# Kernel optimization log

Hardware: AMD Instinct MI355X
Metric: run time of the kernel (lower is better)

Reference implementation:

```python
import jax, jax.numpy as jnp
import numpy as np

# RadixAttention EXTEND forward: queries over newly-extended tokens attend to
# (a) the full cached prefix KV (non-causal) and (b) the extend-token KV (causal),
# equivalent to attention over concat([prefix, extend]) with a shifted causal mask.

SCALING = 0.08838834764831845  # 1/sqrt(128)


def setup_inputs() -> dict:
    key = jax.random.key(0)
    k1, k2, k3, k4, k5 = jax.random.split(key, 5)
    B, E, P, H, Hk, D = 4, 512, 1536, 32, 8, 128
    return {
        "q": jax.random.normal(k1, (B, E, H, D), dtype=jnp.float32),
        "k": jax.random.normal(k2, (B, E, Hk, D), dtype=jnp.float32),
        "v": jax.random.normal(k3, (B, E, Hk, D), dtype=jnp.float32),
        "k_cache": jax.random.normal(k4, (B, P, Hk, D), dtype=jnp.float32),
        "v_cache": jax.random.normal(k5, (B, P, Hk, D), dtype=jnp.float32),
    }


def reference(q, k, v, k_cache, v_cache):
    B, E, H, D = q.shape
    Hk = k.shape[2]
    P = k_cache.shape[1]
    g = H // Hk  # GQA group size
    S = P + E

    k_all = jnp.concatenate([k_cache, k], axis=1)  # [B, S, Hk, D]
    v_all = jnp.concatenate([v_cache, v], axis=1)  # [B, S, Hk, D]

    qg = q.reshape(B, E, Hk, g, D)
    # scores: [B, Hk, g, E, S]
    scores = jnp.einsum("bekgd,bskd->bkges", qg, k_all) * SCALING

    # key j visible to extend-query e iff j <= P + e (prefix fully visible, extend causal)
    visible = jnp.arange(S)[None, :] <= (P + jnp.arange(E))[:, None]  # [E, S]
    scores = jnp.where(visible[None, None, None, :, :], scores, jnp.float32(-1e30))

    p = jax.nn.softmax(scores, axis=-1)
    o = jnp.einsum("bkges,bskd->bekgd", p, v_all).reshape(B, E, H, D)
    # module returns flat [num_tokens, H*D]
    return o.reshape(B * E, H * D)
```

## Files before the change

kernel.cpp:

```cpp
#include <hip/hip_runtime.h>
#include <hip/hip_bf16.h>
#include <stdint.h>
#include <stddef.h>


#define B_ 4
#define E_ 512
#define P_ 1536
#define H_ 32
#define HK_ 8
#define D_ 128
#define G_ 4
#define S_ 2048

#define BLOCK_E 32
#define NT 64
#define PPITCH 72
#define TPITCH 72
#define KVSTRIDE (HK_ * D_)
#define NTHREADS 256
#define M_FIX 12.0f
#define TILE_SHORTS 8192

typedef __attribute__((ext_vector_type(8))) short short8v;
typedef __attribute__((ext_vector_type(4))) float floatx4;

__device__ __forceinline__ short2 f2bf2(float a, float b) {
  __hip_bfloat162 h = __float22bfloat162_rn(float2{a, b});
  return *(short2*)&h;
}
__device__ __forceinline__ short f2bf(float f) {
  union { float f; uint32_t u; } x; x.f = f;
  uint32_t r = x.u + 0x7FFFu + ((x.u >> 16) & 1u);
  return (short)(r >> 16);
}
__device__ __forceinline__ short8v cvt8(const float4 a, const float4 b) {
  short2 p0 = f2bf2(a.x, a.y), p1 = f2bf2(a.z, a.w);
  short2 p2 = f2bf2(b.x, b.y), p3 = f2bf2(b.z, b.w);
  short8v f;
  f[0] = p0.x; f[1] = p0.y; f[2] = p1.x; f[3] = p1.y;
  f[4] = p2.x; f[5] = p2.y; f[6] = p3.x; f[7] = p3.y;
  return f;
}

__global__ __launch_bounds__(256)
void prep_kv(const float* __restrict__ kc, const float* __restrict__ ke,
             const float* __restrict__ vc, const float* __restrict__ ve,
             short* __restrict__ kb, short* __restrict__ vt) {
  __shared__ short TT[D_ * TPITCH];
  const int bid = blockIdx.x;
  const int tid = threadIdx.x;
  if (bid < 4096) {
    const int cid = bid * 256 + tid;
    const int cl  = cid & 15;
    const int j   = (cid >> 4) & (S_ - 1);
    const int kh  = (cid >> 15) & 7;
    const int b   = cid >> 18;
    const float* src = (j < P_)
        ? (kc + (((size_t)b * P_ + j) * HK_ + kh) * D_ + cl * 8)
        : (ke + (((size_t)b * E_ + (j - P_)) * HK_ + kh) * D_ + cl * 8);
    const float4 x0 = *(const float4*)src;
    const float4 x1 = *(const float4*)(src + 4);
    const int t = j >> 6, key = j & 63;
    const int cs = ((cl & 7) ^ (key & 7)) | (cl & 8);
    *(short8v*)&kb[(((size_t)(b * 8 + kh) * 32 + t)) * TILE_SHORTS + key * 128 + cs * 8] =
        cvt8(x0, x1);
  } else {
    const int b2 = bid - 4096;
    const int j0 = (b2 & 31) * 64;
    const int kh = (b2 >> 5) & 7;
    const int b  = b2 >> 8;
#pragma unroll
    for (int it = 0; it < 8; ++it) {
      const int linear = it * 256 + tid;
      const int key = linear >> 5;
      const int dof = (linear & 31) * 4;
      const int j = j0 + key;
      const float* src = (j < P_)
          ? (vc + (((size_t)b * P_ + j) * HK_ + kh) * D_ + dof)
          : (ve + (((size_t)b * E_ + (j - P_)) * HK_ + kh) * D_ + dof);
      const float4 x = *(const float4*)src;
      short2 a = f2bf2(x.x, x.y), c = f2bf2(x.z, x.w);
      TT[(dof + 0) * TPITCH + key] = a.x;
      TT[(dof + 1) * TPITCH + key] = a.y;
      TT[(dof + 2) * TPITCH + key] = c.x;
      TT[(dof + 3) * TPITCH + key] = c.y;
    }
    __syncthreads();
#pragma unroll
    for (int it = 0; it < 4; ++it) {
      const int linear = it * 256 + tid;
      const int d  = linear >> 3;
      const int ck = linear & 7;
      const int cks = ck ^ (d & 7);
      *(short8v*)&vt[(((size_t)(b * 8 + kh) * 32 + (j0 >> 6))) * TILE_SHORTS + d * 64 + cks * 8] =
          *(const short8v*)&TT[d * TPITCH + ck * 8];
    }
  }
}

__global__ __launch_bounds__(NTHREADS, 2)
void radix_attn(const float* __restrict__ q,
                const short* __restrict__ kb,
                const short* __restrict__ vt,
                float* __restrict__ out) {
  __shared__ short KT[2][NT * D_];
  __shared__ short VTs[2][D_ * NT];
  __shared__ short PW[4][16 * PPITCH];

  const int flat = blockIdx.x;
  const int kh   = flat & 7;
  const int b    = (flat >> 3) & 3;
  const int e0   = (flat >> 5) * BLOCK_E;
  const int tid  = threadIdx.x;
  const int wave = tid >> 6;
  const int lane = tid & 63;
  const int quad = lane >> 4;
  const int l16  = lane & 15;
  const int h    = kh * G_ + wave;

  short8v qf[2][4];
#pragma unroll
  for (int rb = 0; rb < 2; ++rb) {
    const int e = e0 + rb * 16 + l16;
    const float* qp = q + (((size_t)b * E_ + e) * H_ + h) * D_ + quad * 8;
#pragma unroll
    for (int kcc = 0; kcc < 4; ++kcc)
      qf[rb][kcc] = cvt8(*(const float4*)(qp + kcc * 32), *(const float4*)(qp + kcc * 32 + 4));
  }

  short8v ones8;
#pragma unroll
  for (int i = 0; i < 8; ++i) ones8[i] = (l16 == 0) ? (short)0x3F80 : (short)0;

  floatx4 oacc[2][8];
#pragma unroll
  for (int rb = 0; rb < 2; ++rb)
#pragma unroll
    for (int dt = 0; dt < 8; ++dt) oacc[rb][dt] = (floatx4){0.f, 0.f, 0.f, 0.f};
  floatx4 acc_l[2] = {(floatx4){0.f, 0.f, 0.f, 0.f}, (floatx4){0.f, 0.f, 0.f, 0.f}};

  const short* kbt = kb + (size_t)(b * 8 + kh) * 32 * TILE_SHORTS;
  const short* vtt = vt + (size_t)(b * 8 + kh) * 32 * TILE_SHORTS;

  const int slimit = P_ + e0 + BLOCK_E;
  const int ntiles = (slimit + NT - 1) / NT;
  const float sc = 0.08838834764831845f * 1.44269504088896340f;

  auto dma = [&](int t, int buf) {
    const char* kg = (const char*)kbt + (size_t)t * 16384 + wave * 4096 + lane * 16;
    const char* vg = (const char*)vtt + (size_t)t * 16384 + wave * 4096 + lane * 16;
    short* kl = &KT[buf][wave * 2048];
    short* vl = &VTs[buf][wave * 2048];
#pragma unroll
    for (int g = 0; g < 4; ++g) {
      __builtin_amdgcn_global_load_lds(
          (const __attribute__((address_space(1))) void*)(kg + g * 1024),
          (__attribute__((address_space(3))) void*)(kl + g * 512), 16, 0, 0);
      __builtin_amdgcn_global_load_lds(
          (const __attribute__((address_space(1))) void*)(vg + g * 1024),
          (__attribute__((address_space(3))) void*)(vl + g * 512), 16, 0, 0);
    }
  };

  dma(0, 0);

  for (int t = 0; t < ntiles; ++t) {
    const int kt0 = t * NT;
    const int cur = t & 1;

    __syncthreads();
    if (t + 1 < ntiles) dma(t + 1, cur ^ 1);

    floatx4 sfr[2][4];
#pragma unroll
    for (int nc = 0; nc < 4; ++nc) {
      short8v kf[4];
#pragma unroll
      for (int kcc = 0; kcc < 4; ++kcc) {
        const int cl = kcc * 4 + quad;
        const int cs = ((cl & 7) ^ (l16 & 7)) | (cl & 8);
        kf[kcc] = *(const short8v*)&KT[cur][(nc * 16 + l16) * D_ + cs * 8];
      }
#pragma unroll
      for (int rb = 0; rb < 2; ++rb) {
        floatx4 acc = (floatx4){0.f, 0.f, 0.f, 0.f};
#pragma unroll
        for (int kcc = 0; kcc < 4; ++kcc)
          acc = __builtin_amdgcn_mfma_f32_16x16x32_bf16(kf[kcc], qf[rb][kcc], acc, 0, 0, 0);
        sfr[rb][nc] = acc;
      }
    }

    short8v vfr[2][4];
#pragma unroll
    for (int kc = 0; kc < 2; ++kc)
#pragma unroll
      for (int dt = 0; dt < 4; ++dt) {
        const int cs = (kc * 4 + quad) ^ (l16 & 7);
        vfr[kc][dt] = *(const short8v*)&VTs[cur][(dt * 16 + l16) * NT + cs * 8];
      }

    short8v pf[2][2];
#pragma unroll
    for (int rb = 0; rb < 2; ++rb) {
      const bool need_mask = (kt0 + NT - 1 > P_ + e0 + rb * 16);
      const int qlim = P_ + e0 + rb * 16 + l16;
#pragma unroll
      for (int nc = 0; nc < 4; ++nc) {
        float p[4];
#pragma unroll
        for (int reg = 0; reg < 4; ++reg) {
          float pe = __builtin_amdgcn_exp2f(__builtin_fmaf(sfr[rb][nc][reg], sc, -M_FIX));
          if (need_mask) {
            const int jkey = kt0 + nc * 16 + quad * 4 + reg;
            if (jkey > qlim) pe = 0.f;
          }
          p[reg] = pe;
        }
        const short2 a = f2bf2(p[0], p[1]), c = f2bf2(p[2], p[3]);
        short4 y; y.x = a.x; y.y = a.y; y.z = c.x; y.w = c.y;
        *(short4*)&PW[wave][l16 * PPITCH + nc * 16 + quad * 4] = y;
      }
#pragma unroll
      for (int kc = 0; kc < 2; ++kc)
        pf[rb][kc] = *(const short8v*)&PW[wave][l16 * PPITCH + kc * 32 + quad * 8];
    }

#pragma unroll
    for (int kc = 0; kc < 2; ++kc) {
#pragma unroll
      for (int dt = 0; dt < 8; ++dt) {
        short8v vf;
        if (dt < 4) {
          vf = vfr[kc][dt];
        } else {
          const int cs = (kc * 4 + quad) ^ (l16 & 7);
          vf = *(const short8v*)&VTs[cur][(dt * 16 + l16) * NT + cs * 8];
        }
#pragma unroll
        for (int rb = 0; rb < 2; ++rb)
          oacc[rb][dt] = __builtin_amdgcn_mfma_f32_16x16x32_bf16(pf[rb][kc], vf, oacc[rb][dt], 0, 0, 0);
      }
#pragma unroll
      for (int rb = 0; rb < 2; ++rb)
        acc_l[rb] = __builtin_amdgcn_mfma_f32_16x16x32_bf16(pf[rb][kc], ones8, acc_l[rb], 0, 0, 0);
    }
  }

#pragma unroll
  for (int rb = 0; rb < 2; ++rb) {
    float inv[4];
#pragma unroll
    for (int reg = 0; reg < 4; ++reg) {
      const float l = __shfl(acc_l[rb][reg], lane & 48, 64);
      inv[reg] = 1.0f / l;
    }
#pragma unroll
    for (int reg = 0; reg < 4; ++reg) {
      const int erow = e0 + rb * 16 + quad * 4 + reg;
      float* op = out + (size_t)(b * E_ + erow) * (H_ * D_) + h * D_ + l16;
#pragma unroll
      for (int dt = 0; dt < 8; ++dt)
        op[dt * 16] = oacc[rb][dt][reg] * inv[reg];
    }
  }
}

__global__ __launch_bounds__(1024, 4)
void radix_attn_fp32(const float* __restrict__ q,
                     const float* __restrict__ ke,
                     const float* __restrict__ ve,
                     const float* __restrict__ kc,
                     const float* __restrict__ vc,
                     float* __restrict__ out) {
  __shared__ short KT[NT * 136];
  __shared__ short VTs[D_ * TPITCH];
  __shared__ short PW[16][16 * 80];
  const int flat = blockIdx.x;
  const int kh = flat & 7, b = (flat >> 3) & 3, e0 = (flat >> 5) * 64;
  const int tid = threadIdx.x, wave = tid >> 6, lane = tid & 63;
  const int quad = lane >> 4, l16 = lane & 15;
  const int gi = wave & 3, rbw = wave >> 2, h = kh * G_ + gi;
  short8v qf[4];
  {
    const int e = e0 + rbw * 16 + l16;
    const float* qp = q + (((size_t)b * E_ + e) * H_ + h) * D_ + quad * 8;
#pragma unroll
    for (int kcc = 0; kcc < 4; ++kcc)
      qf[kcc] = cvt8(*(const float4*)(qp + kcc * 32), *(const float4*)(qp + kcc * 32 + 4));
  }
  short8v ones8;
#pragma unroll
  for (int i = 0; i < 8; ++i) ones8[i] = (l16 == 0) ? (short)0x3F80 : (short)0;
  floatx4 oacc[8];
#pragma unroll
  for (int d = 0; d < 8; ++d) oacc[d] = (floatx4){0.f, 0.f, 0.f, 0.f};
  floatx4 acc_l = (floatx4){0.f, 0.f, 0.f, 0.f};
  float mrow[4];
#pragma unroll
  for (int r = 0; r < 4; ++r) mrow[r] = -1e30f;
  const float* kcb = kc + (size_t)b * P_ * KVSTRIDE + (size_t)kh * D_;
  const float* keb = ke + (size_t)b * E_ * KVSTRIDE + (size_t)kh * D_;
  const float* vcb = vc + (size_t)b * P_ * KVSTRIDE + (size_t)kh * D_;
  const float* veb = ve + (size_t)b * E_ * KVSTRIDE + (size_t)kh * D_;
  const int ntiles = (P_ + e0 + 64) / NT;
  const float sc = 0.08838834764831845f * 1.44269504088896340f;
  for (int t = 0; t < ntiles; ++t) {
    const int kt0 = t * NT;
    __syncthreads();
#pragma unroll
    for (int it = 0; it < 2; ++it) {
      const int linear = it * 1024 + tid;
      const int key = linear >> 5, dof = (linear & 31) * 4;
      const int j = kt0 + key;
      const float* src = (j < P_) ? (kcb + (size_t)j * KVSTRIDE) : (keb + (size_t)(j - P_) * KVSTRIDE);
      const float4 x = *(const float4*)(src + dof);
      short2 a = f2bf2(x.x, x.y), c = f2bf2(x.z, x.w);
      short4 y; y.x = a.x; y.y = a.y; y.z = c.x; y.w = c.y;
      *(short4*)&KT[key * 136 + dof] = y;
    }
#pragma unroll
    for (int it = 0; it < 2; ++it) {
      const int linear = it * 1024 + tid;
      const int key = linear & 63, dg = (linear >> 6) * 4;
      const int j = kt0 + key;
      const float* src = (j < P_) ? (vcb + (size_t)j * KVSTRIDE) : (veb + (size_t)(j - P_) * KVSTRIDE);
      const float4 x = *(const float4*)(src + dg);
      short2 a = f2bf2(x.x, x.y), c = f2bf2(x.z, x.w);
      VTs[(dg + 0) * TPITCH + key] = a.x;
      VTs[(dg + 1) * TPITCH + key] = a.y;
      VTs[(dg + 2) * TPITCH + key] = c.x;
      VTs[(dg + 3) * TPITCH + key] = c.y;
    }
    __syncthreads();
    floatx4 sfr[4];
#pragma unroll
    for (int nc = 0; nc < 4; ++nc) {
      floatx4 acc = (floatx4){0.f, 0.f, 0.f, 0.f};
#pragma unroll
      for (int kcc = 0; kcc < 4; ++kcc) {
        const short8v bf = *(const short8v*)&KT[(nc * 16 + l16) * 136 + kcc * 32 + quad * 8];
        acc = __builtin_amdgcn_mfma_f32_16x16x32_bf16(qf[kcc], bf, acc, 0, 0, 0);
      }
      sfr[nc] = acc;
    }
    const bool need_mask = (kt0 + NT - 1 > P_ + e0 + rbw * 16);
#pragma unroll
    for (int nc = 0; nc < 4; ++nc)
#pragma unroll
      for (int reg = 0; reg < 4; ++reg) {
        float s = sfr[nc][reg] * sc;
        if (need_mask) {
          const int jkey = kt0 + nc * 16 + l16;
          const int erow = e0 + rbw * 16 + quad * 4 + reg;
          if (jkey > P_ + erow) s = -1e30f;
        }
        sfr[nc][reg] = s;
      }
    float mt[4];
#pragma unroll
    for (int reg = 0; reg < 4; ++reg)
      mt[reg] = fmaxf(fmaxf(sfr[0][reg], sfr[1][reg]), fmaxf(sfr[2][reg], sfr[3][reg]));
#pragma unroll
    for (int off = 1; off < 16; off <<= 1)
#pragma unroll
      for (int reg = 0; reg < 4; ++reg)
        mt[reg] = fmaxf(mt[reg], __shfl_xor(mt[reg], off, 64));
#pragma unroll
    for (int reg = 0; reg < 4; ++reg) {
      const float mnew = fmaxf(mrow[reg], mt[reg]);
      const float alpha = __builtin_amdgcn_exp2f(mrow[reg] - mnew);
      mrow[reg] = mnew;
      acc_l[reg] *= alpha;
#pragma unroll
      for (int d = 0; d < 8; ++d) oacc[d][reg] *= alpha;
    }
#pragma unroll
    for (int nc = 0; nc < 4; ++nc)
#pragma unroll
      for (int reg = 0; reg < 4; ++reg) {
        const float p = __builtin_amdgcn_exp2f(sfr[nc][reg] - mrow[reg]);
        PW[wave][(quad * 4 + reg) * 80 + nc * 16 + l16] = f2bf(p);
      }
    const short8v pf0 = *(const short8v*)&PW[wave][l16 * 80 + quad * 8];
    const short8v pf1 = *(const short8v*)&PW[wave][l16 * 80 + 32 + quad * 8];
#pragma unroll
    for (int d = 0; d < 8; ++d) {
      const short8v vf0 = *(const short8v*)&VTs[(d * 16 + l16) * TPITCH + quad * 8];
      const short8v vf1 = *(const short8v*)&VTs[(d * 16 + l16) * TPITCH + 32 + quad * 8];
      oacc[d] = __builtin_amdgcn_mfma_f32_16x16x32_bf16(pf0, vf0, oacc[d], 0, 0, 0);
      oacc[d] = __builtin_amdgcn_mfma_f32_16x16x32_bf16(pf1, vf1, oacc[d], 0, 0, 0);
    }
    acc_l = __builtin_amdgcn_mfma_f32_16x16x32_bf16(pf0, ones8, acc_l, 0, 0, 0);
    acc_l = __builtin_amdgcn_mfma_f32_16x16x32_bf16(pf1, ones8, acc_l, 0, 0, 0);
  }
  float inv[4];
#pragma unroll
  for (int reg = 0; reg < 4; ++reg)
    inv[reg] = 1.0f / __shfl(acc_l[reg], lane & 48, 64);
#pragma unroll
  for (int reg = 0; reg < 4; ++reg) {
    const int erow = e0 + rbw * 16 + quad * 4 + reg;
    float* op = out + (size_t)(b * E_ + erow) * (H_ * D_) + h * D_ + l16;
#pragma unroll
    for (int d = 0; d < 8; ++d)
      op[d * 16] = oacc[d][reg] * inv[reg];
  }
}

extern "C" void kernel_launch(void* const* d_in, const int* in_sizes, int n_in,
                              void* d_out, int out_size, void* d_ws, size_t ws_size,
                              hipStream_t stream) {
  const float* q  = (const float*)d_in[0];
  const float* ke = (const float*)d_in[1];
  const float* ve = (const float*)d_in[2];
  const float* kc = (const float*)d_in[3];
  const float* vc = (const float*)d_in[4];
  float* out = (float*)d_out;

  const size_t kv_shorts = (size_t)B_ * HK_ * S_ * D_;
  const size_t need = 2 * kv_shorts * sizeof(short);

  if (ws_size >= need) {
    short* kb = (short*)d_ws;
    short* vt = kb + kv_shorts;
    prep_kv<<<dim3(4096 + 1024), dim3(256), 0, stream>>>(kc, ke, vc, ve, kb, vt);
    const int nblk = (E_ / BLOCK_E) * HK_ * B_;
    radix_attn<<<dim3(nblk), dim3(NTHREADS), 0, stream>>>(q, kb, vt, out);
  } else {
    radix_attn_fp32<<<dim3(8 * 8 * 4), dim3(1024), 0, stream>>>(q, ke, ve, kc, vc, out);
  }
}
```

Measured before the change: 213.6 us.

## Split row blocks across 8 waves per block and swizzle P scratch

Doubles the block to 512 threads so each wave handles one head and one 16-row slice instead of two slices. This halves per-wave accumulator registers so more waves can be resident (launch bound raised to 4). It also spreads the K/V DMA over 8 waves, XOR-swizzles the P staging buffer instead of padding it, adds s_setprio around the MFMA sections, and unrolls the tile loop by two so the buffer index is a compile-time constant. In exchange, each K fragment loaded from LDS now feeds only one row block, which doubles LDS read traffic per MFMA.

```diff
diff --git a/kernel.cpp b/kernel.cpp
--- a/kernel.cpp
+++ b/kernel.cpp
@@ -15,10 +15,9 @@
 
 #define BLOCK_E 32
 #define NT 64
-#define PPITCH 72
 #define TPITCH 72
 #define KVSTRIDE (HK_ * D_)
-#define NTHREADS 256
+#define NTHREADS 512
 #define M_FIX 12.0f
 #define TILE_SHORTS 8192
 
@@ -99,14 +98,14 @@
   }
 }
 
-__global__ __launch_bounds__(NTHREADS, 2)
+__global__ __launch_bounds__(NTHREADS, 4)
 void radix_attn(const float* __restrict__ q,
                 const short* __restrict__ kb,
                 const short* __restrict__ vt,
                 float* __restrict__ out) {
   __shared__ short KT[2][NT * D_];
   __shared__ short VTs[2][D_ * NT];
-  __shared__ short PW[4][16 * PPITCH];
+  __shared__ short PW[8][1024];
 
   const int flat = blockIdx.x;
   const int kh   = flat & 7;
@@ -117,28 +116,27 @@
   const int lane = tid & 63;
   const int quad = lane >> 4;
   const int l16  = lane & 15;
-  const int h    = kh * G_ + wave;
-
-  short8v qf[2][4];
-#pragma unroll
-  for (int rb = 0; rb < 2; ++rb) {
+  const int gi   = wave & 3;
+  const int rb   = wave >> 2;
+  const int h    = kh * G_ + gi;
+
+  short8v qf[4];
+  {
     const int e = e0 + rb * 16 + l16;
     const float* qp = q + (((size_t)b * E_ + e) * H_ + h) * D_ + quad * 8;
 #pragma unroll
     for (int kcc = 0; kcc < 4; ++kcc)
-      qf[rb][kcc] = cvt8(*(const float4*)(qp + kcc * 32), *(const float4*)(qp + kcc * 32 + 4));
+      qf[kcc] = cvt8(*(const float4*)(qp + kcc * 32), *(const float4*)(qp + kcc * 32 + 4));
   }
 
   short8v ones8;
 #pragma unroll
   for (int i = 0; i < 8; ++i) ones8[i] = (l16 == 0) ? (short)0x3F80 : (short)0;
 
-  floatx4 oacc[2][8];
-#pragma unroll
-  for (int rb = 0; rb < 2; ++rb)
-#pragma unroll
-    for (int dt = 0; dt < 8; ++dt) oacc[rb][dt] = (floatx4){0.f, 0.f, 0.f, 0.f};
-  floatx4 acc_l[2] = {(floatx4){0.f, 0.f, 0.f, 0.f}, (floatx4){0.f, 0.f, 0.f, 0.f}};
+  floatx4 oacc[8];
+#pragma unroll
+  for (int dt = 0; dt < 8; ++dt) oacc[dt] = (floatx4){0.f, 0.f, 0.f, 0.f};
+  floatx4 acc_l = (floatx4){0.f, 0.f, 0.f, 0.f};
 
   const short* kbt = kb + (size_t)(b * 8 + kh) * 32 * TILE_SHORTS;
   const short* vtt = vt + (size_t)(b * 8 + kh) * 32 * TILE_SHORTS;
@@ -147,13 +145,17 @@
   const int ntiles = (slimit + NT - 1) / NT;
   const float sc = 0.08838834764831845f * 1.44269504088896340f;
 
+  const int qlim = P_ + e0 + rb * 16 + l16;
+  const int pb   = l16 * 64;
+  const int swz  = l16 & 7;
+
   auto dma = [&](int t, int buf) {
-    const char* kg = (const char*)kbt + (size_t)t * 16384 + wave * 4096 + lane * 16;
-    const char* vg = (const char*)vtt + (size_t)t * 16384 + wave * 4096 + lane * 16;
-    short* kl = &KT[buf][wave * 2048];
-    short* vl = &VTs[buf][wave * 2048];
-#pragma unroll
-    for (int g = 0; g < 4; ++g) {
+    const char* kg = (const char*)kbt + (size_t)t * 16384 + wave * 2048 + lane * 16;
+    const char* vg = (const char*)vtt + (size_t)t * 16384 + wave * 2048 + lane * 16;
+    short* kl = &KT[buf][wave * 1024];
+    short* vl = &VTs[buf][wave * 1024];
+#pragma unroll
+    for (int g = 0; g < 2; ++g) {
       __builtin_amdgcn_global_load_lds(
           (const __attribute__((address_space(1))) void*)(kg + g * 1024),
           (__attribute__((address_space(3))) void*)(kl + g * 512), 16, 0, 0);
@@ -163,107 +165,101 @@
     }
   };
 
-  dma(0, 0);
-
-  for (int t = 0; t < ntiles; ++t) {
+  auto tile = [&](int t, int cur) {
     const int kt0 = t * NT;
-    const int cur = t & 1;
 
     __syncthreads();
     if (t + 1 < ntiles) dma(t + 1, cur ^ 1);
 
-    floatx4 sfr[2][4];
+    floatx4 sfr[4];
+    __builtin_amdgcn_s_setprio(1);
 #pragma unroll
     for (int nc = 0; nc < 4; ++nc) {
       short8v kf[4];
 #pragma unroll
       for (int kcc = 0; kcc < 4; ++kcc) {
         const int cl = kcc * 4 + quad;
-        const int cs = ((cl & 7) ^ (l16 & 7)) | (cl & 8);
+        const int cs = ((cl & 7) ^ swz) | (cl & 8);
         kf[kcc] = *(const short8v*)&KT[cur][(nc * 16 + l16) * D_ + cs * 8];
       }
-#pragma unroll
-      for (int rb = 0; rb < 2; ++rb) {
-        floatx4 acc = (floatx4){0.f, 0.f, 0.f, 0.f};
-#pragma unroll
-        for (int kcc = 0; kcc < 4; ++kcc)
-          acc = __builtin_amdgcn_mfma_f32_16x16x32_bf16(kf[kcc], qf[rb][kcc], acc, 0, 0, 0);
-        sfr[rb][nc] = acc;
-      }
-    }
-
-    short8v vfr[2][4];
+      floatx4 acc = (floatx4){0.f, 0.f, 0.f, 0.f};
+#pragma unroll
+      for (int kcc = 0; kcc < 4; ++kcc)
+        acc = __builtin_amdgcn_mfma_f32_16x16x32_bf16(kf[kcc], qf[kcc], acc, 0, 0, 0);
+      sfr[nc] = acc;
+    }
+    __builtin_amdgcn_s_setprio(0);
+
+    short8v vfr[4];
+#pragma unroll
+    for (int dt = 0; dt < 4; ++dt) {
+      const int cs = quad ^ swz;
+      vfr[dt] = *(const short8v*)&VTs[cur][(dt * 16 + l16) * NT + cs * 8];
+    }
+
+    const bool need_mask = (kt0 + NT - 1 > P_ + e0 + rb * 16);
+#pragma unroll
+    for (int nc = 0; nc < 4; ++nc) {
+      float p[4];
+#pragma unroll
+      for (int reg = 0; reg < 4; ++reg) {
+        float pe = __builtin_amdgcn_exp2f(__builtin_fmaf(sfr[nc][reg], sc, -M_FIX));
+        if (need_mask) {
+          const int jkey = kt0 + nc * 16 + quad * 4 + reg;
+          if (jkey > qlim) pe = 0.f;
+        }
+        p[reg] = pe;
+      }
+      const short2 a = f2bf2(p[0], p[1]), c = f2bf2(p[2], p[3]);
+      short4 y; y.x = a.x; y.y = a.y; y.z = c.x; y.w = c.y;
+      const int ch = (nc * 2 + (quad >> 1)) ^ swz;
+      *(short4*)&PW[wave][pb + ch * 8 + (quad & 1) * 4] = y;
+    }
+    short8v pf[2];
 #pragma unroll
     for (int kc = 0; kc < 2; ++kc)
-#pragma unroll
-      for (int dt = 0; dt < 4; ++dt) {
-        const int cs = (kc * 4 + quad) ^ (l16 & 7);
-        vfr[kc][dt] = *(const short8v*)&VTs[cur][(dt * 16 + l16) * NT + cs * 8];
-      }
-
-    short8v pf[2][2];
-#pragma unroll
-    for (int rb = 0; rb < 2; ++rb) {
-      const bool need_mask = (kt0 + NT - 1 > P_ + e0 + rb * 16);
-      const int qlim = P_ + e0 + rb * 16 + l16;
-#pragma unroll
-      for (int nc = 0; nc < 4; ++nc) {
-        float p[4];
-#pragma unroll
-        for (int reg = 0; reg < 4; ++reg) {
-          float pe = __builtin_amdgcn_exp2f(__builtin_fmaf(sfr[rb][nc][reg], sc, -M_FIX));
-          if (need_mask) {
-            const int jkey = kt0 + nc * 16 + quad * 4 + reg;
-            if (jkey > qlim) pe = 0.f;
-          }
-          p[reg] = pe;
-        }
-        const short2 a = f2bf2(p[0], p[1]), c = f2bf2(p[2], p[3]);
-        short4 y; y.x = a.x; y.y = a.y; y.z = c.x; y.w = c.y;
-        *(short4*)&PW[wave][l16 * PPITCH + nc * 16 + quad * 4] = y;
-      }
-#pragma unroll
-      for (int kc = 0; kc < 2; ++kc)
-        pf[rb][kc] = *(const short8v*)&PW[wave][l16 * PPITCH + kc * 32 + quad * 8];
-    }
-
+      pf[kc] = *(const short8v*)&PW[wave][pb + ((kc * 4 + quad) ^ swz) * 8];
+
+    __builtin_amdgcn_s_setprio(1);
 #pragma unroll
     for (int kc = 0; kc < 2; ++kc) {
 #pragma unroll
       for (int dt = 0; dt < 8; ++dt) {
         short8v vf;
-        if (dt < 4) {
-          vf = vfr[kc][dt];
+        if (kc == 0 && dt < 4) {
+          vf = vfr[dt];
         } else {
-          const int cs = (kc * 4 + quad) ^ (l16 & 7);
+          const int cs = (kc * 4 + quad) ^ swz;
           vf = *(const short8v*)&VTs[cur][(dt * 16 + l16) * NT + cs * 8];
         }
-#pragma unroll
-        for (int rb = 0; rb < 2; ++rb)
-          oacc[rb][dt] = __builtin_amdgcn_mfma_f32_16x16x32_bf16(pf[rb][kc], vf, oacc[rb][dt], 0, 0, 0);
-      }
-#pragma unroll
-      for (int rb = 0; rb < 2; ++rb)
-        acc_l[rb] = __builtin_amdgcn_mfma_f32_16x16x32_bf16(pf[rb][kc], ones8, acc_l[rb], 0, 0, 0);
-    }
-  }
-
-#pragma unroll
-  for (int rb = 0; rb < 2; ++rb) {
-    float inv[4];
-#pragma unroll
-    for (int reg = 0; reg < 4; ++reg) {
-      const float l = __shfl(acc_l[rb][reg], lane & 48, 64);
-      inv[reg] = 1.0f / l;
-    }
-#pragma unroll
-    for (int reg = 0; reg < 4; ++reg) {
-      const int erow = e0 + rb * 16 + quad * 4 + reg;
-      float* op = out + (size_t)(b * E_ + erow) * (H_ * D_) + h * D_ + l16;
-#pragma unroll
-      for (int dt = 0; dt < 8; ++dt)
-        op[dt * 16] = oacc[rb][dt][reg] * inv[reg];
-    }
+        oacc[dt] = __builtin_amdgcn_mfma_f32_16x16x32_bf16(pf[kc], vf, oacc[dt], 0, 0, 0);
+      }
+      acc_l = __builtin_amdgcn_mfma_f32_16x16x32_bf16(pf[kc], ones8, acc_l, 0, 0, 0);
+    }
+    __builtin_amdgcn_s_setprio(0);
+  };
+
+  dma(0, 0);
+  int t = 0;
+  for (; t + 2 <= ntiles; t += 2) {
+    tile(t, 0);
+    tile(t + 1, 1);
+  }
+  if (t < ntiles) tile(t, 0);
+
+  float inv[4];
+#pragma unroll
+  for (int reg = 0; reg < 4; ++reg) {
+    const float l = __shfl(acc_l[reg], lane & 48, 64);
+    inv[reg] = 1.0f / l;
+  }
+#pragma unroll
+  for (int reg = 0; reg < 4; ++reg) {
+    const int erow = e0 + rb * 16 + quad * 4 + reg;
+    float* op = out + (size_t)(b * E_ + erow) * (H_ * D_) + h * D_ + l16;
+#pragma unroll
+    for (int dt = 0; dt < 8; ++dt)
+      op[dt * 16] = oacc[dt][reg] * inv[reg];
   }
 }
 
```

Result: slower. 218.7 us (+2.4%).

## Split each KV tile across two wave groups with smem reduction of partial outputs

Applied to the files above, without the earlier changes.

Doubles the block to 512 threads so each head's four waves are duplicated, with each half handling 32 of the 64 keys per tile. Partial O and row-sum accumulators are merged through a shared-memory union at the end. The change also adds s_setprio around the MFMA sections and unrolls the tile loop by two to fix buffer indices. The aim is more waves per CU and shorter per-wave dependency chains, at the cost of an extra reduction pass and a larger shared-memory footprint.

```diff
diff --git a/kernel.cpp b/kernel.cpp
--- a/kernel.cpp
+++ b/kernel.cpp
@@ -15,12 +15,13 @@
 
 #define BLOCK_E 32
 #define NT 64
-#define PPITCH 72
 #define TPITCH 72
 #define KVSTRIDE (HK_ * D_)
-#define NTHREADS 256
+#define NTHREADS 512
 #define M_FIX 12.0f
 #define TILE_SHORTS 8192
+#define PP32 40
+#define OPITCH 132
 
 typedef __attribute__((ext_vector_type(8))) short short8v;
 typedef __attribute__((ext_vector_type(4))) float floatx4;
@@ -99,14 +100,22 @@
   }
 }
 
-__global__ __launch_bounds__(NTHREADS, 2)
+__global__ __launch_bounds__(NTHREADS, 4)
 void radix_attn(const float* __restrict__ q,
                 const short* __restrict__ kb,
                 const short* __restrict__ vt,
                 float* __restrict__ out) {
-  __shared__ short KT[2][NT * D_];
-  __shared__ short VTs[2][D_ * NT];
-  __shared__ short PW[4][16 * PPITCH];
+  __shared__ union SMemU {
+    struct {
+      short KT[2][NT * D_];
+      short VTs[2][D_ * NT];
+      short PW[8][16 * PP32];
+    } a;
+    struct {
+      float Ob[4][32][OPITCH];
+      float Lb[4][32];
+    } r;
+  } smem;
 
   const int flat = blockIdx.x;
   const int kh   = flat & 7;
@@ -117,7 +126,9 @@
   const int lane = tid & 63;
   const int quad = lane >> 4;
   const int l16  = lane & 15;
-  const int h    = kh * G_ + wave;
+  const int gi   = wave & 3;
+  const int kx   = wave >> 2;
+  const int h    = kh * G_ + gi;
 
   short8v qf[2][4];
 #pragma unroll
@@ -147,13 +158,17 @@
   const int ntiles = (slimit + NT - 1) / NT;
   const float sc = 0.08838834764831845f * 1.44269504088896340f;
 
+  const int swz = l16 & 7;
+  const int csv = (kx * 4 + quad) ^ swz;
+  const int pb  = l16 * PP32;
+
   auto dma = [&](int t, int buf) {
-    const char* kg = (const char*)kbt + (size_t)t * 16384 + wave * 4096 + lane * 16;
-    const char* vg = (const char*)vtt + (size_t)t * 16384 + wave * 4096 + lane * 16;
-    short* kl = &KT[buf][wave * 2048];
-    short* vl = &VTs[buf][wave * 2048];
-#pragma unroll
-    for (int g = 0; g < 4; ++g) {
+    const char* kg = (const char*)kbt + (size_t)t * 16384 + wave * 2048 + lane * 16;
+    const char* vg = (const char*)vtt + (size_t)t * 16384 + wave * 2048 + lane * 16;
+    short* kl = &smem.a.KT[buf][wave * 1024];
+    short* vl = &smem.a.VTs[buf][wave * 1024];
+#pragma unroll
+    for (int g = 0; g < 2; ++g) {
       __builtin_amdgcn_global_load_lds(
           (const __attribute__((address_space(1))) void*)(kg + g * 1024),
           (__attribute__((address_space(3))) void*)(kl + g * 512), 16, 0, 0);
@@ -163,24 +178,24 @@
     }
   };
 
-  dma(0, 0);
-
-  for (int t = 0; t < ntiles; ++t) {
+  auto tile = [&](int t, int cur) {
     const int kt0 = t * NT;
-    const int cur = t & 1;
+    const int k0  = kt0 + kx * 32;
 
     __syncthreads();
     if (t + 1 < ntiles) dma(t + 1, cur ^ 1);
 
-    floatx4 sfr[2][4];
-#pragma unroll
-    for (int nc = 0; nc < 4; ++nc) {
+    floatx4 sfr[2][2];
+    __builtin_amdgcn_s_setprio(1);
+#pragma unroll
+    for (int nc = 0; nc < 2; ++nc) {
       short8v kf[4];
+      const int keyrow = kx * 32 + nc * 16 + l16;
 #pragma unroll
       for (int kcc = 0; kcc < 4; ++kcc) {
         const int cl = kcc * 4 + quad;
-        const int cs = ((cl & 7) ^ (l16 & 7)) | (cl & 8);
-        kf[kcc] = *(const short8v*)&KT[cur][(nc * 16 + l16) * D_ + cs * 8];
+        const int cs = ((cl & 7) ^ swz) | (cl & 8);
+        kf[kcc] = *(const short8v*)&smem.a.KT[cur][keyrow * D_ + cs * 8];
       }
 #pragma unroll
       for (int rb = 0; rb < 2; ++rb) {
@@ -191,78 +206,91 @@
         sfr[rb][nc] = acc;
       }
     }
-
-    short8v vfr[2][4];
-#pragma unroll
-    for (int kc = 0; kc < 2; ++kc)
-#pragma unroll
-      for (int dt = 0; dt < 4; ++dt) {
-        const int cs = (kc * 4 + quad) ^ (l16 & 7);
-        vfr[kc][dt] = *(const short8v*)&VTs[cur][(dt * 16 + l16) * NT + cs * 8];
-      }
-
-    short8v pf[2][2];
+    __builtin_amdgcn_s_setprio(0);
+
+    short8v pf[2];
 #pragma unroll
     for (int rb = 0; rb < 2; ++rb) {
-      const bool need_mask = (kt0 + NT - 1 > P_ + e0 + rb * 16);
+      const bool need_mask = (k0 + 31 > P_ + e0 + rb * 16);
       const int qlim = P_ + e0 + rb * 16 + l16;
 #pragma unroll
-      for (int nc = 0; nc < 4; ++nc) {
+      for (int nc = 0; nc < 2; ++nc) {
         float p[4];
 #pragma unroll
         for (int reg = 0; reg < 4; ++reg) {
           float pe = __builtin_amdgcn_exp2f(__builtin_fmaf(sfr[rb][nc][reg], sc, -M_FIX));
           if (need_mask) {
-            const int jkey = kt0 + nc * 16 + quad * 4 + reg;
+            const int jkey = k0 + nc * 16 + quad * 4 + reg;
             if (jkey > qlim) pe = 0.f;
           }
           p[reg] = pe;
         }
         const short2 a = f2bf2(p[0], p[1]), c = f2bf2(p[2], p[3]);
         short4 y; y.x = a.x; y.y = a.y; y.z = c.x; y.w = c.y;
-        *(short4*)&PW[wave][l16 * PPITCH + nc * 16 + quad * 4] = y;
-      }
-#pragma unroll
-      for (int kc = 0; kc < 2; ++kc)
-        pf[rb][kc] = *(const short8v*)&PW[wave][l16 * PPITCH + kc * 32 + quad * 8];
-    }
-
-#pragma unroll
-    for (int kc = 0; kc < 2; ++kc) {
-#pragma unroll
-      for (int dt = 0; dt < 8; ++dt) {
-        short8v vf;
-        if (dt < 4) {
-          vf = vfr[kc][dt];
-        } else {
-          const int cs = (kc * 4 + quad) ^ (l16 & 7);
-          vf = *(const short8v*)&VTs[cur][(dt * 16 + l16) * NT + cs * 8];
-        }
-#pragma unroll
-        for (int rb = 0; rb < 2; ++rb)
-          oacc[rb][dt] = __builtin_amdgcn_mfma_f32_16x16x32_bf16(pf[rb][kc], vf, oacc[rb][dt], 0, 0, 0);
-      }
+        *(short4*)&smem.a.PW[wave][pb + nc * 16 + quad * 4] = y;
+      }
+      pf[rb] = *(const short8v*)&smem.a.PW[wave][pb + quad * 8];
+    }
+
+    __builtin_amdgcn_s_setprio(1);
+#pragma unroll
+    for (int dt = 0; dt < 8; ++dt) {
+      const short8v vf = *(const short8v*)&smem.a.VTs[cur][(dt * 16 + l16) * NT + csv * 8];
 #pragma unroll
       for (int rb = 0; rb < 2; ++rb)
-        acc_l[rb] = __builtin_amdgcn_mfma_f32_16x16x32_bf16(pf[rb][kc], ones8, acc_l[rb], 0, 0, 0);
-    }
-  }
-
-#pragma unroll
-  for (int rb = 0; rb < 2; ++rb) {
-    float inv[4];
-#pragma unroll
-    for (int reg = 0; reg < 4; ++reg) {
-      const float l = __shfl(acc_l[rb][reg], lane & 48, 64);
-      inv[reg] = 1.0f / l;
-    }
-#pragma unroll
-    for (int reg = 0; reg < 4; ++reg) {
-      const int erow = e0 + rb * 16 + quad * 4 + reg;
-      float* op = out + (size_t)(b * E_ + erow) * (H_ * D_) + h * D_ + l16;
+        oacc[rb][dt] = __builtin_amdgcn_mfma_f32_16x16x32_bf16(pf[rb], vf, oacc[rb][dt], 0, 0, 0);
+    }
+#pragma unroll
+    for (int rb = 0; rb < 2; ++rb)
+      acc_l[rb] = __builtin_amdgcn_mfma_f32_16x16x32_bf16(pf[rb], ones8, acc_l[rb], 0, 0, 0);
+    __builtin_amdgcn_s_setprio(0);
+  };
+
+  dma(0, 0);
+  int t = 0;
+  for (; t + 2 <= ntiles; t += 2) {
+    tile(t, 0);
+    tile(t + 1, 1);
+  }
+  if (t < ntiles) tile(t, 0);
+
+  __syncthreads();
+  if (kx == 1) {
+#pragma unroll
+    for (int rb = 0; rb < 2; ++rb)
 #pragma unroll
       for (int dt = 0; dt < 8; ++dt)
-        op[dt * 16] = oacc[rb][dt][reg] * inv[reg];
+#pragma unroll
+        for (int reg = 0; reg < 4; ++reg)
+          smem.r.Ob[gi][rb * 16 + quad * 4 + reg][dt * 16 + l16] = oacc[rb][dt][reg];
+    if (l16 == 0) {
+#pragma unroll
+      for (int rb = 0; rb < 2; ++rb)
+#pragma unroll
+        for (int reg = 0; reg < 4; ++reg)
+          smem.r.Lb[gi][rb * 16 + quad * 4 + reg] = acc_l[rb][reg];
+    }
+  }
+  __syncthreads();
+  if (kx == 0) {
+#pragma unroll
+    for (int rb = 0; rb < 2; ++rb) {
+      float inv[4];
+#pragma unroll
+      for (int reg = 0; reg < 4; ++reg) {
+        const int row = rb * 16 + quad * 4 + reg;
+        const float l = __shfl(acc_l[rb][reg], lane & 48, 64) + smem.r.Lb[gi][row];
+        inv[reg] = 1.0f / l;
+      }
+#pragma unroll
+      for (int reg = 0; reg < 4; ++reg) {
+        const int row = rb * 16 + quad * 4 + reg;
+        const int erow = e0 + row;
+        float* op = out + (size_t)(b * E_ + erow) * (H_ * D_) + h * D_ + l16;
+#pragma unroll
+        for (int dt = 0; dt < 8; ++dt)
+          op[dt * 16] = (oacc[rb][dt][reg] + smem.r.Ob[gi][row][dt * 16 + l16]) * inv[reg];
+      }
     }
   }
 }
```

Measured after the change: 523.5 us. 2.45x slower.

## Read V tiles directly from global memory and drop V shared buffers

Applied to the files above, without the earlier changes.

V tiles are no longer staged in shared memory through async global-to-LDS copies. Each wave now reads its bf16 V fragments straight from global memory, and the XOR swizzle is removed from the V pre-pack kernel. This frees LDS so occupancy can rise to 3 blocks per CU, and the loop is restructured with score and softmax fused per chunk, wave priority hints around the MFMA sections, and an unroll by two to get static buffer indices. The cost is that V loads now carry global/L2 latency inside the PV loop with no prefetch, and the four waves of a block each re-read the same V tile.

```diff
diff --git a/kernel.cpp b/kernel.cpp
--- a/kernel.cpp
+++ b/kernel.cpp
@@ -15,12 +15,12 @@
 
 #define BLOCK_E 32
 #define NT 64
-#define PPITCH 72
 #define TPITCH 72
 #define KVSTRIDE (HK_ * D_)
 #define NTHREADS 256
 #define M_FIX 12.0f
 #define TILE_SHORTS 8192
+#define PPITCH 72
 
 typedef __attribute__((ext_vector_type(8))) short short8v;
 typedef __attribute__((ext_vector_type(4))) float floatx4;
@@ -92,21 +92,19 @@
       const int linear = it * 256 + tid;
       const int d  = linear >> 3;
       const int ck = linear & 7;
-      const int cks = ck ^ (d & 7);
-      *(short8v*)&vt[(((size_t)(b * 8 + kh) * 32 + (j0 >> 6))) * TILE_SHORTS + d * 64 + cks * 8] =
+      *(short8v*)&vt[(((size_t)(b * 8 + kh) * 32 + (j0 >> 6))) * TILE_SHORTS + d * 64 + ck * 8] =
           *(const short8v*)&TT[d * TPITCH + ck * 8];
     }
   }
 }
 
-__global__ __launch_bounds__(NTHREADS, 2)
+__global__ __launch_bounds__(NTHREADS, 3)
 void radix_attn(const float* __restrict__ q,
                 const short* __restrict__ kb,
                 const short* __restrict__ vt,
                 float* __restrict__ out) {
   __shared__ short KT[2][NT * D_];
-  __shared__ short VTs[2][D_ * NT];
-  __shared__ short PW[4][16 * PPITCH];
+  __shared__ short PW[4][32 * PPITCH];
 
   const int flat = blockIdx.x;
   const int kh   = flat & 7;
@@ -147,39 +145,34 @@
   const int ntiles = (slimit + NT - 1) / NT;
   const float sc = 0.08838834764831845f * 1.44269504088896340f;
 
+  const int swz = l16 & 7;
+  const int pwrow = l16 * PPITCH;
+
   auto dma = [&](int t, int buf) {
     const char* kg = (const char*)kbt + (size_t)t * 16384 + wave * 4096 + lane * 16;
-    const char* vg = (const char*)vtt + (size_t)t * 16384 + wave * 4096 + lane * 16;
     short* kl = &KT[buf][wave * 2048];
-    short* vl = &VTs[buf][wave * 2048];
 #pragma unroll
     for (int g = 0; g < 4; ++g) {
       __builtin_amdgcn_global_load_lds(
           (const __attribute__((address_space(1))) void*)(kg + g * 1024),
           (__attribute__((address_space(3))) void*)(kl + g * 512), 16, 0, 0);
-      __builtin_amdgcn_global_load_lds(
-          (const __attribute__((address_space(1))) void*)(vg + g * 1024),
-          (__attribute__((address_space(3))) void*)(vl + g * 512), 16, 0, 0);
     }
   };
 
-  dma(0, 0);
-
-  for (int t = 0; t < ntiles; ++t) {
+  auto tile = [&](int t, int cur) {
     const int kt0 = t * NT;
-    const int cur = t & 1;
 
     __syncthreads();
     if (t + 1 < ntiles) dma(t + 1, cur ^ 1);
 
-    floatx4 sfr[2][4];
+    __builtin_amdgcn_s_setprio(1);
 #pragma unroll
     for (int nc = 0; nc < 4; ++nc) {
       short8v kf[4];
 #pragma unroll
       for (int kcc = 0; kcc < 4; ++kcc) {
         const int cl = kcc * 4 + quad;
-        const int cs = ((cl & 7) ^ (l16 & 7)) | (cl & 8);
+        const int cs = ((cl & 7) ^ swz) | (cl & 8);
         kf[kcc] = *(const short8v*)&KT[cur][(nc * 16 + l16) * D_ + cs * 8];
       }
 #pragma unroll
@@ -188,30 +181,12 @@
 #pragma unroll
         for (int kcc = 0; kcc < 4; ++kcc)
           acc = __builtin_amdgcn_mfma_f32_16x16x32_bf16(kf[kcc], qf[rb][kcc], acc, 0, 0, 0);
-        sfr[rb][nc] = acc;
-      }
-    }
-
-    short8v vfr[2][4];
-#pragma unroll
-    for (int kc = 0; kc < 2; ++kc)
-#pragma unroll
-      for (int dt = 0; dt < 4; ++dt) {
-        const int cs = (kc * 4 + quad) ^ (l16 & 7);
-        vfr[kc][dt] = *(const short8v*)&VTs[cur][(dt * 16 + l16) * NT + cs * 8];
-      }
-
-    short8v pf[2][2];
-#pragma unroll
-    for (int rb = 0; rb < 2; ++rb) {
-      const bool need_mask = (kt0 + NT - 1 > P_ + e0 + rb * 16);
-      const int qlim = P_ + e0 + rb * 16 + l16;
-#pragma unroll
-      for (int nc = 0; nc < 4; ++nc) {
+        const bool need_mask = (kt0 + NT - 1 > P_ + e0 + rb * 16);
+        const int qlim = P_ + e0 + rb * 16 + l16;
         float p[4];
 #pragma unroll
         for (int reg = 0; reg < 4; ++reg) {
-          float pe = __builtin_amdgcn_exp2f(__builtin_fmaf(sfr[rb][nc][reg], sc, -M_FIX));
+          float pe = __builtin_amdgcn_exp2f(__builtin_fmaf(acc[reg], sc, -M_FIX));
           if (need_mask) {
             const int jkey = kt0 + nc * 16 + quad * 4 + reg;
             if (jkey > qlim) pe = 0.f;
@@ -220,33 +195,37 @@
         }
         const short2 a = f2bf2(p[0], p[1]), c = f2bf2(p[2], p[3]);
         short4 y; y.x = a.x; y.y = a.y; y.z = c.x; y.w = c.y;
-        *(short4*)&PW[wave][l16 * PPITCH + nc * 16 + quad * 4] = y;
-      }
-#pragma unroll
-      for (int kc = 0; kc < 2; ++kc)
-        pf[rb][kc] = *(const short8v*)&PW[wave][l16 * PPITCH + kc * 32 + quad * 8];
-    }
-
-#pragma unroll
-    for (int kc = 0; kc < 2; ++kc) {
+        *(short4*)&PW[wave][(rb * 16 + l16) * PPITCH + nc * 16 + quad * 4] = y;
+      }
+    }
+    __builtin_amdgcn_s_setprio(0);
+
+    const short* vb = vtt + (size_t)t * TILE_SHORTS;
+#pragma unroll
+    for (int rb = 0; rb < 2; ++rb) {
+      const short8v pf0 = *(const short8v*)&PW[wave][(rb * 16 + l16) * PPITCH + quad * 8];
+      const short8v pf1 = *(const short8v*)&PW[wave][(rb * 16 + l16) * PPITCH + 32 + quad * 8];
+      __builtin_amdgcn_s_setprio(1);
 #pragma unroll
       for (int dt = 0; dt < 8; ++dt) {
-        short8v vf;
-        if (dt < 4) {
-          vf = vfr[kc][dt];
-        } else {
-          const int cs = (kc * 4 + quad) ^ (l16 & 7);
-          vf = *(const short8v*)&VTs[cur][(dt * 16 + l16) * NT + cs * 8];
-        }
-#pragma unroll
-        for (int rb = 0; rb < 2; ++rb)
-          oacc[rb][dt] = __builtin_amdgcn_mfma_f32_16x16x32_bf16(pf[rb][kc], vf, oacc[rb][dt], 0, 0, 0);
-      }
-#pragma unroll
-      for (int rb = 0; rb < 2; ++rb)
-        acc_l[rb] = __builtin_amdgcn_mfma_f32_16x16x32_bf16(pf[rb][kc], ones8, acc_l[rb], 0, 0, 0);
-    }
-  }
+        const short8v vf0 = *(const short8v*)&vb[(dt * 16 + l16) * 64 + quad * 8];
+        const short8v vf1 = *(const short8v*)&vb[(dt * 16 + l16) * 64 + 32 + quad * 8];
+        oacc[rb][dt] = __builtin_amdgcn_mfma_f32_16x16x32_bf16(pf0, vf0, oacc[rb][dt], 0, 0, 0);
+        oacc[rb][dt] = __builtin_amdgcn_mfma_f32_16x16x32_bf16(pf1, vf1, oacc[rb][dt], 0, 0, 0);
+      }
+      acc_l[rb] = __builtin_amdgcn_mfma_f32_16x16x32_bf16(pf0, ones8, acc_l[rb], 0, 0, 0);
+      acc_l[rb] = __builtin_amdgcn_mfma_f32_16x16x32_bf16(pf1, ones8, acc_l[rb], 0, 0, 0);
+      __builtin_amdgcn_s_setprio(0);
+    }
+  };
+
+  dma(0, 0);
+  int t = 0;
+  for (; t + 2 <= ntiles; t += 2) {
+    tile(t, 0);
+    tile(t + 1, 1);
+  }
+  if (t < ntiles) tile(t, 0);
 
 #pragma unroll
   for (int rb = 0; rb < 2; ++rb) {
```

Result: slower. 489.3 us (+129.1%).
